# Kernel optimization log

Hardware: AMD Instinct MI355X
Metric: run time of the kernel (lower is better)

## Reference

```python
import jax, jax.numpy as jnp
import numpy as np

B, CIN, COUT, H, W, K, SDIM = 16, 256, 256, 64, 64, 3, 128

def setup_inputs() -> dict:
    key = jax.random.key(0)
    ks = jax.random.split(key, 5)
    return {
        "x": jax.random.normal(ks[0], (B, CIN, H, W), dtype=jnp.float32),
        "c_src": jax.random.normal(ks[1], (B, SDIM), dtype=jnp.float32),
        "c_trg": jax.random.normal(ks[2], (B, SDIM), dtype=jnp.float32),
        "style_w": jax.random.normal(ks[3], (CIN, SDIM), dtype=jnp.float32),
        "style_b": jnp.ones((CIN,), dtype=jnp.float32),  # bias_init=1
        "weight": jax.random.normal(ks[4], (1, COUT, CIN, K, K), dtype=jnp.float32),
    }

def reference(x, c_src, c_trg, style_w, style_b, weight):
    b, cin, h, w = x.shape
    _, cout, _, k, _ = weight.shape
    # EqualLinear: scale = 1/sqrt(dim_in)=1/sqrt(128), lr_mul=1
    lin_scale = np.float32(1.0 / np.sqrt(SDIM))
    s = c_trg @ (style_w * lin_scale).T + style_b            # [B, Cin]
    # modulate
    conv_scale = np.float32(1.0 / np.sqrt(cin * k * k))
    wmod = conv_scale * weight * s[:, None, :, None, None]   # [B, Cout, Cin, K, K]
    # demodulate
    demod = jax.lax.rsqrt(jnp.sum(wmod * wmod, axis=(2, 3, 4)) + 1e-8)  # [B, Cout]
    wmod = wmod * demod[:, :, None, None, None]
    # grouped conv with groups=batch == per-sample conv; vmap over batch
    def conv_one(xb, wb):
        # xb: [Cin,H,W], wb: [Cout,Cin,K,K]
        return jax.lax.conv_general_dilated(
            xb[None], wb, window_strides=(1, 1), padding="SAME",
            dimension_numbers=("NCHW", "OIHW", "NCHW"))[0]
    out = jax.vmap(conv_one)(x, wmod)                        # [B, Cout, H, W]
    return out
```

## Files before the change

### kernel.cpp

```cpp
#include <hip/hip_runtime.h>


#define WSH_OFF    35684352
#define S_OFF      36864000
#define G_OFF      36880384
#define DEMOD_OFF  37142528

typedef __attribute__((ext_vector_type(8))) short bf16x8;
typedef __attribute__((ext_vector_type(4))) float f32x4;
typedef __attribute__((ext_vector_type(4))) int i32x4;

#define GLOAD_LDS16(g, l)                                                        \
  __builtin_amdgcn_global_load_lds(                                              \
      (const __attribute__((address_space(1))) void*)(g),                        \
      (__attribute__((address_space(3))) void*)(l), 16, 0, 0)

__device__ __forceinline__ unsigned short f2bf(float f) {
  unsigned int u = __builtin_bit_cast(unsigned int, f);
  u += 0x7FFFu + ((u >> 16) & 1u);
  return (unsigned short)(u >> 16);
}

__global__ void prep1_k(const float* __restrict__ c_trg,
                        const float* __restrict__ style_w,
                        const float* __restrict__ style_b,
                        const float* __restrict__ weight,
                        float* __restrict__ s,
                        short* __restrict__ wsh,
                        float* __restrict__ G) {
  const int blk = blockIdx.x;
  const int tid = threadIdx.x;
  if (blk < 16) {
    const int b = blk;
    const float* ct = c_trg + b * 128;
    const float* sw = style_w + tid * 128;
    float acc = 0.f;
#pragma unroll 4
    for (int d = 0; d < 128; ++d) acc += ct[d] * sw[d];
    s[b * 256 + tid] = acc * 0.08838834764831845f + style_b[tid];
  } else {
    const int idx = (blk - 16) * 256 + tid;
    const float* wsrc = weight + idx * 9;
    float g = 0.f;
#pragma unroll
    for (int t = 0; t < 9; ++t) {
      float v = wsrc[t] * 0.020833333333333332f;
      g += v * v;
      wsh[t * 65536 + idx] = (short)f2bf(v);
    }
    G[idx] = g;
  }
}

__global__ void xpose_k(const float* __restrict__ x,
                        const float* __restrict__ s,
                        const float* __restrict__ G,
                        short* __restrict__ xpad,
                        float* __restrict__ demod) {
  __shared__ float tile[64][65];
  const int bid = blockIdx.x;
  const int tid = threadIdx.x;
  if (bid >= 4112) {
    const int id = bid - 4112;
    const int b = id >> 8, co = id & 255;
    const float sv = s[b * 256 + tid];
    float ss = G[co * 256 + tid] * sv * sv;
#pragma unroll
    for (int o = 32; o; o >>= 1) ss += __shfl_down(ss, o);
    __shared__ float red[4];
    if ((tid & 63) == 0) red[tid >> 6] = ss;
    __syncthreads();
    if (tid == 0) demod[id] = rsqrtf(red[0] + red[1] + red[2] + red[3] + 1e-8f);
    return;
  }
  if (bid >= 4096) {
    const int b = bid - 4096;
    char* base = (char*)xpad + b * 66 * 66 * 512;
    const i32x4 z = {0, 0, 0, 0};
    for (int i = tid; i < 4224; i += 256) {
      const int r = i >= 2112;
      const int off = r * (65 * 66 * 512) + (i - r * 2112) * 16;
      *(i32x4*)(base + off) = z;
    }
    for (int i = tid; i < 4096; i += 256) {
      const int h = 1 + (i >> 6);
      const int side = (i >> 5) & 1;
      const int j = i & 31;
      *(i32x4*)(base + (h * 66 + side * 65) * 512 + j * 16) = z;
    }
    return;
  }
  const int ct = bid & 3;
  const int h = (bid >> 2) & 63;
  const int b = bid >> 8;
  const int w = tid & 63, cl = tid >> 6;
  const float* src = x + ((b * 256 + ct * 64) * 64 + h) * 64;
#pragma unroll
  for (int i = 0; i < 16; ++i) {
    int c = i * 4 + cl;
    tile[c][w] = src[c * 4096 + w];
  }
  const int cp = tid & 31;
  const float s0 = s[b * 256 + ct * 64 + cp * 2];
  const float s1 = s[b * 256 + ct * 64 + cp * 2 + 1];
  __syncthreads();
  short* dst = xpad + ((b * 66 + h + 1) * 66 + 1) * 256 + ct * 64;
#pragma unroll
  for (int i = 0; i < 8; ++i) {
    int idx = i * 256 + tid;
    int w2 = idx >> 5;
    unsigned int u = (unsigned int)f2bf(tile[cp * 2][w2] * s0) |
                     ((unsigned int)f2bf(tile[cp * 2 + 1][w2] * s1) << 16);
    *(unsigned int*)(dst + w2 * 256 + cp * 2) = u;
  }
}

__global__ __launch_bounds__(512, 2) void conv_k(const short* __restrict__ xpad,
                                                 const short* __restrict__ wsh,
                                                 const float* __restrict__ demod,
                                                 float* __restrict__ out) {
  extern __shared__ __align__(16) char lds[];

  const int tid = threadIdx.x;
  const int lane = tid & 63;
  const int wid = tid >> 6;
  const int wm = wid >> 2;
  const int wn = wid & 3;

  const int orig = blockIdx.x;
  const int bid = (orig & 7) * 32 + (orig >> 3);
  const int b = bid >> 4;
  const int r0 = (bid & 15) * 4;

  const int t3 = tid >> 3;
  const int c16 = (tid & 7) * 16;
  const int swzc = c16 ^ ((t3 & 7) << 4);
  int aO[4], bO[4];
#pragma unroll
  for (int j = 0; j < 4; ++j) {
    aO[j] = (j * 64 + t3) * 512 + swzc;
    bO[j] = ((b * 66 + r0 + j) * 66 + t3) * 512 + swzc;
  }
  const char* wB = (const char*)wsh;
  const char* xB = (const char*)xpad;

  auto stageA = [&](int ts) {
    const int tap = ts >> 2, cc = ts & 3;
    const int aAdd = tap * 131072 + cc * 128;
    char* d = lds + (ts & 1) * 65536;
#pragma unroll
    for (int j = 0; j < 4; ++j)
      GLOAD_LDS16(wB + aAdd + aO[j], d + j * 8192 + tid * 16);
  };
  auto stageB = [&](int ts) {
    const int tap = ts >> 2, cc = ts & 3;
    const int dh = (tap * 11) >> 5;
    const int bAdd = (dh * 66 + (tap - dh * 3)) * 512 + cc * 128;
    char* d = lds + (ts & 1) * 65536 + 32768;
#pragma unroll
    for (int j = 0; j < 4; ++j)
      GLOAD_LDS16(xB + bAdd + bO[j], d + j * 8192 + tid * 16);
  };

  const int xall = (lane & 7) << 4;
  const int xl = xall & 0x30;
  const int xh = xall & 0x40;
  const int colR = (((lane >> 4) << 4) ^ xl);
  const int ko0 = xh;
  const int ko1 = 64 ^ xh;
  const int aRdBase = (wm * 128 + (lane & 15)) * 128 + colR;
  const int bRdBase = 32768 + (wn * 64 + (lane & 15)) * 128 + colR;

  f32x4 acc[8][4] = {};

  stageA(0);
  stageB(0);

  for (int t = 0; t < 36; ++t) {
    asm volatile("s_waitcnt vmcnt(0)" ::: "memory");
    __builtin_amdgcn_s_barrier();
    __builtin_amdgcn_sched_barrier(0);

    const char* Ab = lds + (t & 1) * 65536 + aRdBase;
    const char* Bb = lds + (t & 1) * 65536 + bRdBase;
    bf16x8 af[4][2], bq[2][2], bq2[2][2];

#pragma unroll
    for (int m = 0; m < 4; ++m) {
      af[m][0] = *(const bf16x8*)(Ab + m * 2048 + ko0);
      af[m][1] = *(const bf16x8*)(Ab + m * 2048 + ko1);
    }
#pragma unroll
    for (int n = 0; n < 2; ++n) {
      bq[n][0] = *(const bf16x8*)(Bb + n * 2048 + ko0);
      bq[n][1] = *(const bf16x8*)(Bb + n * 2048 + ko1);
    }
    if (t + 1 < 36) stageA(t + 1);
    asm volatile("s_waitcnt lgkmcnt(0)" ::: "memory");
    __builtin_amdgcn_sched_barrier(0);
    __builtin_amdgcn_s_setprio(1);
#pragma unroll
    for (int m = 0; m < 4; ++m)
#pragma unroll
      for (int n = 0; n < 2; ++n) {
        acc[m][n] = __builtin_amdgcn_mfma_f32_16x16x32_bf16(af[m][0], bq[n][0], acc[m][n], 0, 0, 0);
        acc[m][n] = __builtin_amdgcn_mfma_f32_16x16x32_bf16(af[m][1], bq[n][1], acc[m][n], 0, 0, 0);
      }
    __builtin_amdgcn_s_setprio(0);

#pragma unroll
    for (int n = 0; n < 2; ++n) {
      bq2[n][0] = *(const bf16x8*)(Bb + (n + 2) * 2048 + ko0);
      bq2[n][1] = *(const bf16x8*)(Bb + (n + 2) * 2048 + ko1);
    }
    if (t + 1 < 36) stageB(t + 1);
    asm volatile("s_waitcnt lgkmcnt(0)" ::: "memory");
    __builtin_amdgcn_sched_barrier(0);
    __builtin_amdgcn_s_setprio(1);
#pragma unroll
    for (int m = 0; m < 4; ++m)
#pragma unroll
      for (int n = 0; n < 2; ++n) {
        acc[m][n + 2] = __builtin_amdgcn_mfma_f32_16x16x32_bf16(af[m][0], bq2[n][0], acc[m][n + 2], 0, 0, 0);
        acc[m][n + 2] = __builtin_amdgcn_mfma_f32_16x16x32_bf16(af[m][1], bq2[n][1], acc[m][n + 2], 0, 0, 0);
      }
    __builtin_amdgcn_s_setprio(0);

#pragma unroll
    for (int m = 0; m < 4; ++m) {
      af[m][0] = *(const bf16x8*)(Ab + (m + 4) * 2048 + ko0);
      af[m][1] = *(const bf16x8*)(Ab + (m + 4) * 2048 + ko1);
    }
    asm volatile("s_waitcnt lgkmcnt(0)" ::: "memory");
    __builtin_amdgcn_sched_barrier(0);
    __builtin_amdgcn_s_setprio(1);
#pragma unroll
    for (int m = 0; m < 4; ++m)
#pragma unroll
      for (int n = 0; n < 2; ++n) {
        acc[m + 4][n] = __builtin_amdgcn_mfma_f32_16x16x32_bf16(af[m][0], bq[n][0], acc[m + 4][n], 0, 0, 0);
        acc[m + 4][n] = __builtin_amdgcn_mfma_f32_16x16x32_bf16(af[m][1], bq[n][1], acc[m + 4][n], 0, 0, 0);
      }
    __builtin_amdgcn_s_setprio(0);

    __builtin_amdgcn_s_setprio(1);
#pragma unroll
    for (int m = 0; m < 4; ++m)
#pragma unroll
      for (int n = 0; n < 2; ++n) {
        acc[m + 4][n + 2] = __builtin_amdgcn_mfma_f32_16x16x32_bf16(af[m][0], bq2[n][0], acc[m + 4][n + 2], 0, 0, 0);
        acc[m + 4][n + 2] = __builtin_amdgcn_mfma_f32_16x16x32_bf16(af[m][1], bq2[n][1], acc[m + 4][n + 2], 0, 0, 0);
      }
    __builtin_amdgcn_s_setprio(0);
    asm volatile("" ::: "memory");
  }

  const int pc = lane & 15;
  const int rOff = (lane >> 4) * 4;
  const int h = r0 + wn;
#pragma unroll
  for (int m = 0; m < 8; ++m) {
#pragma unroll
    for (int r = 0; r < 4; ++r) {
      const int co = wm * 128 + m * 16 + rOff + r;
      const float dm = demod[(b << 8) + co];
      float* orow = out + (((b << 8) + co) << 12) + (h << 6);
#pragma unroll
      for (int n = 0; n < 4; ++n) {
        orow[n * 16 + pc] = acc[m][n][r] * dm;
      }
    }
  }
}

extern "C" void kernel_launch(void* const* d_in, const int* in_sizes, int n_in,
                              void* d_out, int out_size, void* d_ws, size_t ws_size,
                              hipStream_t stream) {
  const float* x       = (const float*)d_in[0];
  const float* c_trg   = (const float*)d_in[2];
  const float* style_w = (const float*)d_in[3];
  const float* style_b = (const float*)d_in[4];
  const float* weight  = (const float*)d_in[5];
  float* out = (float*)d_out;

  char* ws = (char*)d_ws;
  short* xpad  = (short*)(ws);
  short* wsh   = (short*)(ws + WSH_OFF);
  float* s     = (float*)(ws + S_OFF);
  float* G     = (float*)(ws + G_OFF);
  float* demod = (float*)(ws + DEMOD_OFF);

  hipFuncSetAttribute((const void*)conv_k,
                      hipFuncAttributeMaxDynamicSharedMemorySize, 131072);

  prep1_k<<<272, 256, 0, stream>>>(c_trg, style_w, style_b, weight, s, wsh, G);
  xpose_k<<<8208, 256, 0, stream>>>(x, s, G, xpad, demod);
  conv_k<<<256, 512, 131072, stream>>>(xpad, wsh, demod, out);
}
```

Before: 96.47 us.

## Switch conv GEMM inner loop to 32x32x16 bf16 MFMA tiles

Replaces the 16x16x32 MFMA tiling (8x4 accumulator tiles per wave) with 32x32x16 MFMA (4x2 tiles of 16 floats), and reworks the LDS read addressing and swizzle to match the new operand layout. Larger MFMA tiles need fewer LDS operand reads per FLOP and fewer instructions. The explicit lgkmcnt waits and sched barriers between phases are also dropped, leaving the compiler to order LDS reads and MFMAs. This risks changed bank-conflict behaviour, relies on the compiler inserting correct waits, and changes the epilogue's store pattern.

```diff
diff --git a/kernel.cpp b/kernel.cpp
--- a/kernel.cpp
+++ b/kernel.cpp
@@ -7,7 +7,7 @@
 #define DEMOD_OFF  37142528
 
 typedef __attribute__((ext_vector_type(8))) short bf16x8;
-typedef __attribute__((ext_vector_type(4))) float f32x4;
+typedef __attribute__((ext_vector_type(16))) float f32x16;
 typedef __attribute__((ext_vector_type(4))) int i32x4;
 
 #define GLOAD_LDS16(g, l)                                                        \
@@ -162,16 +162,15 @@
       GLOAD_LDS16(xB + bAdd + bO[j], d + j * 8192 + tid * 16);
   };
 
-  const int xall = (lane & 7) << 4;
-  const int xl = xall & 0x30;
-  const int xh = xall & 0x40;
-  const int colR = (((lane >> 4) << 4) ^ xl);
-  const int ko0 = xh;
-  const int ko1 = 64 ^ xh;
-  const int aRdBase = (wm * 128 + (lane & 15)) * 128 + colR;
-  const int bRdBase = 32768 + (wn * 64 + (lane & 15)) * 128 + colR;
-
-  f32x4 acc[8][4] = {};
+  const int xk = (lane & 7) << 4;
+  int colx[4];
+#pragma unroll
+  for (int kk = 0; kk < 4; ++kk)
+    colx[kk] = ((kk * 32) ^ (xk & 0x60)) + (((lane >> 5) << 4) ^ (xk & 16));
+  const int aRdBase = (wm * 128 + (lane & 31)) * 128;
+  const int bRdBase = 32768 + (wn * 64 + (lane & 31)) * 128;
+
+  f32x16 acc[4][2] = {};
 
   stageA(0);
   stageB(0);
@@ -183,91 +182,65 @@
 
     const char* Ab = lds + (t & 1) * 65536 + aRdBase;
     const char* Bb = lds + (t & 1) * 65536 + bRdBase;
-    bf16x8 af[4][2], bq[2][2], bq2[2][2];
-
-#pragma unroll
-    for (int m = 0; m < 4; ++m) {
-      af[m][0] = *(const bf16x8*)(Ab + m * 2048 + ko0);
-      af[m][1] = *(const bf16x8*)(Ab + m * 2048 + ko1);
-    }
-#pragma unroll
-    for (int n = 0; n < 2; ++n) {
-      bq[n][0] = *(const bf16x8*)(Bb + n * 2048 + ko0);
-      bq[n][1] = *(const bf16x8*)(Bb + n * 2048 + ko1);
+    bf16x8 a01[2][4], a23[2][4], b0[4], b1[4];
+
+#pragma unroll
+    for (int kk = 0; kk < 4; ++kk) {
+      a01[0][kk] = *(const bf16x8*)(Ab + 0 * 4096 + colx[kk]);
+      a01[1][kk] = *(const bf16x8*)(Ab + 1 * 4096 + colx[kk]);
+      b0[kk]     = *(const bf16x8*)(Bb + 0 * 4096 + colx[kk]);
     }
     if (t + 1 < 36) stageA(t + 1);
-    asm volatile("s_waitcnt lgkmcnt(0)" ::: "memory");
-    __builtin_amdgcn_sched_barrier(0);
     __builtin_amdgcn_s_setprio(1);
 #pragma unroll
-    for (int m = 0; m < 4; ++m)
-#pragma unroll
-      for (int n = 0; n < 2; ++n) {
-        acc[m][n] = __builtin_amdgcn_mfma_f32_16x16x32_bf16(af[m][0], bq[n][0], acc[m][n], 0, 0, 0);
-        acc[m][n] = __builtin_amdgcn_mfma_f32_16x16x32_bf16(af[m][1], bq[n][1], acc[m][n], 0, 0, 0);
-      }
+    for (int kk = 0; kk < 4; ++kk) {
+      acc[0][0] = __builtin_amdgcn_mfma_f32_32x32x16_bf16(a01[0][kk], b0[kk], acc[0][0], 0, 0, 0);
+      acc[1][0] = __builtin_amdgcn_mfma_f32_32x32x16_bf16(a01[1][kk], b0[kk], acc[1][0], 0, 0, 0);
+    }
     __builtin_amdgcn_s_setprio(0);
 
 #pragma unroll
-    for (int n = 0; n < 2; ++n) {
-      bq2[n][0] = *(const bf16x8*)(Bb + (n + 2) * 2048 + ko0);
-      bq2[n][1] = *(const bf16x8*)(Bb + (n + 2) * 2048 + ko1);
-    }
+    for (int kk = 0; kk < 4; ++kk)
+      b1[kk] = *(const bf16x8*)(Bb + 1 * 4096 + colx[kk]);
     if (t + 1 < 36) stageB(t + 1);
-    asm volatile("s_waitcnt lgkmcnt(0)" ::: "memory");
-    __builtin_amdgcn_sched_barrier(0);
     __builtin_amdgcn_s_setprio(1);
 #pragma unroll
-    for (int m = 0; m < 4; ++m)
-#pragma unroll
-      for (int n = 0; n < 2; ++n) {
-        acc[m][n + 2] = __builtin_amdgcn_mfma_f32_16x16x32_bf16(af[m][0], bq2[n][0], acc[m][n + 2], 0, 0, 0);
-        acc[m][n + 2] = __builtin_amdgcn_mfma_f32_16x16x32_bf16(af[m][1], bq2[n][1], acc[m][n + 2], 0, 0, 0);
-      }
+    for (int kk = 0; kk < 4; ++kk) {
+      acc[0][1] = __builtin_amdgcn_mfma_f32_32x32x16_bf16(a01[0][kk], b1[kk], acc[0][1], 0, 0, 0);
+      acc[1][1] = __builtin_amdgcn_mfma_f32_32x32x16_bf16(a01[1][kk], b1[kk], acc[1][1], 0, 0, 0);
+    }
     __builtin_amdgcn_s_setprio(0);
 
 #pragma unroll
-    for (int m = 0; m < 4; ++m) {
-      af[m][0] = *(const bf16x8*)(Ab + (m + 4) * 2048 + ko0);
-      af[m][1] = *(const bf16x8*)(Ab + (m + 4) * 2048 + ko1);
-    }
-    asm volatile("s_waitcnt lgkmcnt(0)" ::: "memory");
-    __builtin_amdgcn_sched_barrier(0);
+    for (int kk = 0; kk < 4; ++kk) {
+      a23[0][kk] = *(const bf16x8*)(Ab + 2 * 4096 + colx[kk]);
+      a23[1][kk] = *(const bf16x8*)(Ab + 3 * 4096 + colx[kk]);
+    }
     __builtin_amdgcn_s_setprio(1);
 #pragma unroll
-    for (int m = 0; m < 4; ++m)
-#pragma unroll
-      for (int n = 0; n < 2; ++n) {
-        acc[m + 4][n] = __builtin_amdgcn_mfma_f32_16x16x32_bf16(af[m][0], bq[n][0], acc[m + 4][n], 0, 0, 0);
-        acc[m + 4][n] = __builtin_amdgcn_mfma_f32_16x16x32_bf16(af[m][1], bq[n][1], acc[m + 4][n], 0, 0, 0);
-      }
-    __builtin_amdgcn_s_setprio(0);
-
-    __builtin_amdgcn_s_setprio(1);
-#pragma unroll
-    for (int m = 0; m < 4; ++m)
-#pragma unroll
-      for (int n = 0; n < 2; ++n) {
-        acc[m + 4][n + 2] = __builtin_amdgcn_mfma_f32_16x16x32_bf16(af[m][0], bq2[n][0], acc[m + 4][n + 2], 0, 0, 0);
-        acc[m + 4][n + 2] = __builtin_amdgcn_mfma_f32_16x16x32_bf16(af[m][1], bq2[n][1], acc[m + 4][n + 2], 0, 0, 0);
-      }
+    for (int kk = 0; kk < 4; ++kk) {
+      acc[2][0] = __builtin_amdgcn_mfma_f32_32x32x16_bf16(a23[0][kk], b0[kk], acc[2][0], 0, 0, 0);
+      acc[3][0] = __builtin_amdgcn_mfma_f32_32x32x16_bf16(a23[1][kk], b0[kk], acc[3][0], 0, 0, 0);
+      acc[2][1] = __builtin_amdgcn_mfma_f32_32x32x16_bf16(a23[0][kk], b1[kk], acc[2][1], 0, 0, 0);
+      acc[3][1] = __builtin_amdgcn_mfma_f32_32x32x16_bf16(a23[1][kk], b1[kk], acc[3][1], 0, 0, 0);
+    }
     __builtin_amdgcn_s_setprio(0);
     asm volatile("" ::: "memory");
   }
 
-  const int pc = lane & 15;
-  const int rOff = (lane >> 4) * 4;
+  const int w = lane & 31;
+  const int rHi = (lane >> 5) * 4;
   const int h = r0 + wn;
 #pragma unroll
-  for (int m = 0; m < 8; ++m) {
-#pragma unroll
-    for (int r = 0; r < 4; ++r) {
-      const int co = wm * 128 + m * 16 + rOff + r;
-      const float dm = demod[(b << 8) + co];
-      float* orow = out + (((b << 8) + co) << 12) + (h << 6);
-#pragma unroll
-      for (int n = 0; n < 4; ++n) {
-        orow[n * 16 + pc] = acc[m][n][r] * dm;
+  for (int mt = 0; mt < 4; ++mt) {
+#pragma unroll
+    for (int nt = 0; nt < 2; ++nt) {
+      const int ww = nt * 32 + w;
+#pragma unroll
+      for (int r = 0; r < 16; ++r) {
+        const int co = wm * 128 + mt * 32 + (r & 3) + 8 * (r >> 2) + rHi;
+        const float dm = demod[(b << 8) + co];
+        out[((((b << 8) + co) << 12)) + (h << 6) + ww] = acc[mt][nt][r] * dm;
       }
     }
   }
```

Measured after the change: 112.7 us. 16.9% more time.

## Shrink conv tile to 128x128 with 256-thread blocks and 1024-block grid

Applied to the files above, without the earlier changes.

The implicit-GEMM conv tile drops from 256 output channels by 256 pixels (512 threads, 128KB LDS) to 128 channels by 128 pixels (256 threads, 64KB LDS). The grid grows from 256 to 1024 blocks, splitting each sample's work across two cout halves and pairs of rows. This aims to fill all CUs with more blocks and let more workgroups reside per CU. In exchange each block reuses loaded operands less, so global and LDS traffic per FLOP rises.

```diff
diff --git a/kernel.cpp b/kernel.cpp
--- a/kernel.cpp
+++ b/kernel.cpp
@@ -115,7 +115,7 @@
   }
 }
 
-__global__ __launch_bounds__(512, 2) void conv_k(const short* __restrict__ xpad,
+__global__ __launch_bounds__(256, 2) void conv_k(const short* __restrict__ xpad,
                                                  const short* __restrict__ wsh,
                                                  const float* __restrict__ demod,
                                                  float* __restrict__ out) {
@@ -124,13 +124,15 @@
   const int tid = threadIdx.x;
   const int lane = tid & 63;
   const int wid = tid >> 6;
-  const int wm = wid >> 2;
-  const int wn = wid & 3;
+  const int wm = wid >> 1;
+  const int wn = wid & 1;
 
   const int orig = blockIdx.x;
-  const int bid = (orig & 7) * 32 + (orig >> 3);
-  const int b = bid >> 4;
-  const int r0 = (bid & 15) * 4;
+  const int bid = (orig & 7) * 128 + (orig >> 3);
+  const int b = bid >> 6;
+  const int rem = bid & 63;
+  const int cout0 = (rem & 1) * 128;
+  const int r0 = (rem >> 1) * 2;
 
   const int t3 = tid >> 3;
   const int c16 = (tid & 7) * 16;
@@ -138,8 +140,9 @@
   int aO[4], bO[4];
 #pragma unroll
   for (int j = 0; j < 4; ++j) {
-    aO[j] = (j * 64 + t3) * 512 + swzc;
-    bO[j] = ((b * 66 + r0 + j) * 66 + t3) * 512 + swzc;
+    aO[j] = (cout0 + j * 32 + t3) * 512 + swzc;
+    const int p = j * 32 + t3;
+    bO[j] = ((b * 66 + r0 + (p >> 6)) * 66 + (p & 63)) * 512 + swzc;
   }
   const char* wB = (const char*)wsh;
   const char* xB = (const char*)xpad;
@@ -147,19 +150,19 @@
   auto stageA = [&](int ts) {
     const int tap = ts >> 2, cc = ts & 3;
     const int aAdd = tap * 131072 + cc * 128;
-    char* d = lds + (ts & 1) * 65536;
+    char* d = lds + (ts & 1) * 32768;
 #pragma unroll
     for (int j = 0; j < 4; ++j)
-      GLOAD_LDS16(wB + aAdd + aO[j], d + j * 8192 + tid * 16);
+      GLOAD_LDS16(wB + aAdd + aO[j], d + j * 4096 + tid * 16);
   };
   auto stageB = [&](int ts) {
     const int tap = ts >> 2, cc = ts & 3;
     const int dh = (tap * 11) >> 5;
     const int bAdd = (dh * 66 + (tap - dh * 3)) * 512 + cc * 128;
-    char* d = lds + (ts & 1) * 65536 + 32768;
+    char* d = lds + (ts & 1) * 32768 + 16384;
 #pragma unroll
     for (int j = 0; j < 4; ++j)
-      GLOAD_LDS16(xB + bAdd + bO[j], d + j * 8192 + tid * 16);
+      GLOAD_LDS16(xB + bAdd + bO[j], d + j * 4096 + tid * 16);
   };
 
   const int xall = (lane & 7) << 4;
@@ -168,10 +171,10 @@
   const int colR = (((lane >> 4) << 4) ^ xl);
   const int ko0 = xh;
   const int ko1 = 64 ^ xh;
-  const int aRdBase = (wm * 128 + (lane & 15)) * 128 + colR;
-  const int bRdBase = 32768 + (wn * 64 + (lane & 15)) * 128 + colR;
-
-  f32x4 acc[8][4] = {};
+  const int aRdBase = (wm * 64 + (lane & 15)) * 128 + colR;
+  const int bRdBase = 16384 + (wn * 64 + (lane & 15)) * 128 + colR;
+
+  f32x4 acc[4][4] = {};
 
   stageA(0);
   stageB(0);
@@ -181,12 +184,12 @@
     __builtin_amdgcn_s_barrier();
     __builtin_amdgcn_sched_barrier(0);
 
-    const char* Ab = lds + (t & 1) * 65536 + aRdBase;
-    const char* Bb = lds + (t & 1) * 65536 + bRdBase;
+    const char* Ab = lds + (t & 1) * 32768 + aRdBase;
+    const char* Bb = lds + (t & 1) * 32768 + bRdBase;
     bf16x8 af[4][2], bq[2][2], bq2[2][2];
 
 #pragma unroll
-    for (int m = 0; m < 4; ++m) {
+    for (int m = 0; m < 2; ++m) {
       af[m][0] = *(const bf16x8*)(Ab + m * 2048 + ko0);
       af[m][1] = *(const bf16x8*)(Ab + m * 2048 + ko1);
     }
@@ -200,7 +203,7 @@
     __builtin_amdgcn_sched_barrier(0);
     __builtin_amdgcn_s_setprio(1);
 #pragma unroll
-    for (int m = 0; m < 4; ++m)
+    for (int m = 0; m < 2; ++m)
 #pragma unroll
       for (int n = 0; n < 2; ++n) {
         acc[m][n] = __builtin_amdgcn_mfma_f32_16x16x32_bf16(af[m][0], bq[n][0], acc[m][n], 0, 0, 0);
@@ -218,7 +221,7 @@
     __builtin_amdgcn_sched_barrier(0);
     __builtin_amdgcn_s_setprio(1);
 #pragma unroll
-    for (int m = 0; m < 4; ++m)
+    for (int m = 0; m < 2; ++m)
 #pragma unroll
       for (int n = 0; n < 2; ++n) {
         acc[m][n + 2] = __builtin_amdgcn_mfma_f32_16x16x32_bf16(af[m][0], bq2[n][0], acc[m][n + 2], 0, 0, 0);
@@ -227,29 +230,21 @@
     __builtin_amdgcn_s_setprio(0);
 
 #pragma unroll
-    for (int m = 0; m < 4; ++m) {
-      af[m][0] = *(const bf16x8*)(Ab + (m + 4) * 2048 + ko0);
-      af[m][1] = *(const bf16x8*)(Ab + (m + 4) * 2048 + ko1);
+    for (int m = 0; m < 2; ++m) {
+      af[m + 2][0] = *(const bf16x8*)(Ab + (m + 2) * 2048 + ko0);
+      af[m + 2][1] = *(const bf16x8*)(Ab + (m + 2) * 2048 + ko1);
     }
     asm volatile("s_waitcnt lgkmcnt(0)" ::: "memory");
     __builtin_amdgcn_sched_barrier(0);
     __builtin_amdgcn_s_setprio(1);
 #pragma unroll
-    for (int m = 0; m < 4; ++m)
+    for (int m = 0; m < 2; ++m)
 #pragma unroll
       for (int n = 0; n < 2; ++n) {
-        acc[m + 4][n] = __builtin_amdgcn_mfma_f32_16x16x32_bf16(af[m][0], bq[n][0], acc[m + 4][n], 0, 0, 0);
-        acc[m + 4][n] = __builtin_amdgcn_mfma_f32_16x16x32_bf16(af[m][1], bq[n][1], acc[m + 4][n], 0, 0, 0);
-      }
-    __builtin_amdgcn_s_setprio(0);
-
-    __builtin_amdgcn_s_setprio(1);
-#pragma unroll
-    for (int m = 0; m < 4; ++m)
-#pragma unroll
-      for (int n = 0; n < 2; ++n) {
-        acc[m + 4][n + 2] = __builtin_amdgcn_mfma_f32_16x16x32_bf16(af[m][0], bq2[n][0], acc[m + 4][n + 2], 0, 0, 0);
-        acc[m + 4][n + 2] = __builtin_amdgcn_mfma_f32_16x16x32_bf16(af[m][1], bq2[n][1], acc[m + 4][n + 2], 0, 0, 0);
+        acc[m + 2][n] = __builtin_amdgcn_mfma_f32_16x16x32_bf16(af[m + 2][0], bq[n][0], acc[m + 2][n], 0, 0, 0);
+        acc[m + 2][n] = __builtin_amdgcn_mfma_f32_16x16x32_bf16(af[m + 2][1], bq[n][1], acc[m + 2][n], 0, 0, 0);
+        acc[m + 2][n + 2] = __builtin_amdgcn_mfma_f32_16x16x32_bf16(af[m + 2][0], bq2[n][0], acc[m + 2][n + 2], 0, 0, 0);
+        acc[m + 2][n + 2] = __builtin_amdgcn_mfma_f32_16x16x32_bf16(af[m + 2][1], bq2[n][1], acc[m + 2][n + 2], 0, 0, 0);
       }
     __builtin_amdgcn_s_setprio(0);
     asm volatile("" ::: "memory");
@@ -257,17 +252,18 @@
 
   const int pc = lane & 15;
   const int rOff = (lane >> 4) * 4;
-  const int h = r0 + wn;
-#pragma unroll
-  for (int m = 0; m < 8; ++m) {
+#pragma unroll
+  for (int m = 0; m < 4; ++m) {
 #pragma unroll
     for (int r = 0; r < 4; ++r) {
-      const int co = wm * 128 + m * 16 + rOff + r;
+      const int co = cout0 + wm * 64 + m * 16 + rOff + r;
       const float dm = demod[(b << 8) + co];
-      float* orow = out + (((b << 8) + co) << 12) + (h << 6);
+      float* obase = out + (((b << 8) + co) << 12);
 #pragma unroll
       for (int n = 0; n < 4; ++n) {
-        orow[n * 16 + pc] = acc[m][n][r] * dm;
+        const int pix = wn * 64 + n * 16 + pc;
+        const int h = r0 + (pix >> 6), w = pix & 63;
+        obase[(h << 6) + w] = acc[m][n][r] * dm;
       }
     }
   }
@@ -291,9 +287,9 @@
   float* demod = (float*)(ws + DEMOD_OFF);
 
   hipFuncSetAttribute((const void*)conv_k,
-                      hipFuncAttributeMaxDynamicSharedMemorySize, 131072);
+                      hipFuncAttributeMaxDynamicSharedMemorySize, 65536);
 
   prep1_k<<<272, 256, 0, stream>>>(c_trg, style_w, style_b, weight, s, wsh, G);
   xpose_k<<<8208, 256, 0, stream>>>(x, s, G, xpad, demod);
-  conv_k<<<256, 512, 131072, stream>>>(xpad, wsh, demod, out);
-}
+  conv_k<<<1024, 256, 65536, stream>>>(xpad, wsh, demod, out);
+}
```

Measured after the change: 109.1 us. 13.1% more time.
